# Kernel optimization log

Measured on AMD Instinct MI355X. Metric: run time of the kernel, lower is better.

Reference implementation:

```python
import jax, jax.numpy as jnp
import numpy as np
from jax import lax

B, V, N = 32, 3, 128          # batch, views, worm points
H, W = 512, 512               # image_size
DECAY_FACTOR = 10.0           # MAX_DECAY_FACTOR buffer value
OOB = 1e-05                   # oob_grad_val
MAX_STEPS = 10
LR, ALPHA, EPS = 0.2, 0.99, 1e-08  # torch.optim.RMSprop defaults (lr=0.2)

_b = jnp.arange(B)[:, None, None]   # (B,1,1)
_c = jnp.arange(V)[None, :, None]   # (1,3,1)


def _get_yx(p):
    # round -> long -> clamp to [0, H-1]; col 1 is y (row), col 0 is x (col)
    pi = jnp.clip(jnp.round(p).astype(jnp.int32), 0, H - 1)
    return pi[..., 1], pi[..., 0]  # each (B,3,N)


def _points_to_masks(p):
    y, x = _get_yx(p)
    return jnp.zeros((B, V, H, W), jnp.float32).at[_b, _c, y, x].set(1.0)


def _gradient_surface(masks_diff):
    grad0 = -masks_diff  # (B,3,H,W)
    grads = [grad0]
    g = grad0
    while g.shape[-1] > 1:
        gp = jnp.pad(g, ((0, 0), (0, 0), (1, 1), (1, 1)), constant_values=OOB)
        g = lax.reduce_window(gp, 0.0, lax.add, (1, 1, 3, 3), (1, 1, 2, 2), 'VALID') / 9.0
        grads.append(g)
    gs = jnp.zeros_like(grad0)
    for g in grads:
        # F.interpolate bilinear align_corners=False == jax.image.resize 'linear'
        gs = gs + jax.image.resize(g, grad0.shape, 'linear')
    ga = gs / len(grads)
    gapx = jnp.pad(ga, ((0, 0), (0, 0), (1, 1), (0, 0)), mode='edge')
    gx = (gapx[:, :, :-2] - gapx[:, :, 2:]) * 0.5   # central diff along H
    gapy = jnp.pad(ga, ((0, 0), (0, 0), (0, 0), (1, 1)), mode='edge')
    gy = (gapy[..., :-2] - gapy[..., 2:]) * 0.5     # central diff along W
    return jnp.stack([gx, gy])  # (2,B,3,H,W)


def setup_inputs() -> dict:
    key = jax.random.key(0)
    k1, k2 = jax.random.split(key)
    points_2d = jax.random.uniform(k1, (B, V, N, 2), jnp.float32) * (H - 1)
    masks_target = jax.random.uniform(k2, (B, V, H, W), jnp.float32)
    return {'points_2d': points_2d, 'masks_target': masks_target}


def reference(points_2d, masks_target):
    decay = jnp.exp(-jnp.arange(N, dtype=jnp.float32) / N * DECAY_FACTOR)  # (N,)
    masks_out = _points_to_masks(points_2d)
    masks_diff = masks_target - 0.01 * masks_out
    J = _gradient_surface(masks_diff)  # (2,B,3,H,W)
    p0 = lax.stop_gradient(points_2d)  # matches .clone().detach()

    def body(carry, _):
        p, sq, done = carry
        y, x = _get_yx(p)
        pl = (1.0 - masks_target[_b, _c, y, x]) * decay  # (B,3,N)
        cont = pl.max() > 0.1
        active = jnp.logical_and(jnp.logical_not(done), cont)
        gxp = J[0][_b, _c, y, x]
        gyp = J[1][_b, _c, y, x]
        g = -jnp.stack([gyp, gxp], axis=-1) * pl[..., None]  # (B,3,N,2)
        # RMSprop step
        sq_n = ALPHA * sq + (1.0 - ALPHA) * g * g
        p_n = p - LR * g / (jnp.sqrt(sq_n) + EPS)
        p = jnp.where(active, p_n, p)
        sq = jnp.where(active, sq_n, sq)
        done = jnp.logical_or(done, jnp.logical_not(cont))
        return (p, sq, done), None

    (p_opt, _, _), _ = lax.scan(body, (p0, jnp.zeros_like(p0), jnp.array(False)), None, length=MAX_STEPS)
    masks_opt = _points_to_masks(p_opt)
    return masks_out, masks_opt, p_opt
```

## Files before the change

### kernel.cpp

```cpp
#include <hip/hip_runtime.h>

#define IMGS 96
#define HW   262144
#define NPTS 12288
#define OOBV 1e-5f

static constexpr size_t PYR_OFF   = 0;
static constexpr size_t PFIN_OFF  = 8388576;
static constexpr size_t PLMAX_OFF = 8413152;
static constexpr size_t CNT_OFF   = 8413163;
static constexpr size_t LIST_OFF  = 8413164;
static constexpr size_t GA_OFF    = 8425472;

__device__ __forceinline__ int clampi(int v, int lo, int hi) {
    v = v < lo ? lo : v;
    return v > hi ? hi : v;
}

__global__ void k_scatter(const float* __restrict__ pts, float* __restrict__ mo,
                          int* __restrict__ cnt, int* __restrict__ plist) {
    int i = blockIdx.x * blockDim.x + threadIdx.x;
    if (i >= NPTS) return;
    float px = pts[2*i], py = pts[2*i+1];
    int xi = clampi((int)rintf(px), 0, 511);
    int yi = clampi((int)rintf(py), 0, 511);
    int gp = (i >> 7) * HW + yi * 512 + xi;
    float old = atomicExch(&mo[gp], 1.0f);
    if (old == 0.0f) {
        int k = atomicAdd(cnt, 1);
        plist[k] = gp;
    }
}

__global__ void k_lvl1(const float* __restrict__ mt, float* __restrict__ out) {
    int t = blockIdx.x * blockDim.x + threadIdx.x;
    if (t >= IMGS * 65536) return;
    int j = t & 255, i = (t >> 8) & 255, img = t >> 16;
    const float* m = mt + (size_t)img * HW;
    float s = 0.0f;
    #pragma unroll
    for (int dy = -1; dy <= 1; ++dy) {
        int y = 2*i + dy;
        #pragma unroll
        for (int dx = -1; dx <= 1; ++dx) {
            int x = 2*j + dx;
            s += (y >= 0 && y < 512 && x >= 0 && x < 512) ? -m[y*512 + x] : OOBV;
        }
    }
    out[t] = s / 9.0f;
}

__global__ void k_corr1(const int* __restrict__ cnt, const int* __restrict__ plist,
                        float* __restrict__ lvl1) {
    int k = blockIdx.x * blockDim.x + threadIdx.x;
    if (k >= *cnt) return;
    int gp = plist[k];
    int img = gp >> 18;
    int r = gp & (HW - 1);
    int y = r >> 9, x = r & 511;
    float* L = lvl1 + (size_t)img * 65536;
    const float c = 0.01f / 9.0f;
    int ilo = y >> 1, ihi = ((y + 1) >> 1) > 255 ? 255 : ((y + 1) >> 1);
    int jlo = x >> 1, jhi = ((x + 1) >> 1) > 255 ? 255 : ((x + 1) >> 1);
    for (int i = ilo; i <= ihi; ++i)
        for (int j = jlo; j <= jhi; ++j)
            atomicAdd(&L[i*256 + j], c);
}

__global__ void k_lvl2(const float* __restrict__ in, float* __restrict__ out) {
    int t = blockIdx.x * blockDim.x + threadIdx.x;
    if (t >= IMGS * 16384) return;
    int j = t & 127, i = (t >> 7) & 127, img = t >> 14;
    const float* m = in + (size_t)img * 65536;
    float s = 0.0f;
    #pragma unroll
    for (int dy = -1; dy <= 1; ++dy) {
        int y = 2*i + dy;
        #pragma unroll
        for (int dx = -1; dx <= 1; ++dx) {
            int x = 2*j + dx;
            s += (y >= 0 && y < 256 && x >= 0 && x < 256) ? m[y*256 + x] : OOBV;
        }
    }
    out[t] = s / 9.0f;
}

__global__ __launch_bounds__(256) void k_pyrtail(float* __restrict__ pyr) {
    __shared__ float buf[5461];
    int img = blockIdx.x;
    const float* L2 = pyr + 6291456 + (size_t)img * 16384;
    for (int t = threadIdx.x; t < 4096; t += 256) {
        int i = t >> 6, j = t & 63;
        float s = 0.0f;
        #pragma unroll
        for (int dy = -1; dy <= 1; ++dy) {
            int y = 2*i + dy;
            #pragma unroll
            for (int dx = -1; dx <= 1; ++dx) {
                int x = 2*j + dx;
                s += (y >= 0 && y < 128 && x >= 0 && x < 128) ? L2[y*128 + x] : OOBV;
            }
        }
        float v = s / 9.0f;
        buf[t] = v;
        pyr[7864320 + (size_t)img * 4096 + t] = v;
    }
    __syncthreads();
    int inOff = 0, sin = 64;
    size_t goff = 8257536;
    while (sin > 1) {
        int sout = sin >> 1;
        int outOff = inOff + sin * sin;
        for (int t = threadIdx.x; t < sout * sout; t += 256) {
            int i = t / sout, j = t - i * sout;
            float s = 0.0f;
            for (int dy = -1; dy <= 1; ++dy) {
                int y = 2*i + dy;
                for (int dx = -1; dx <= 1; ++dx) {
                    int x = 2*j + dx;
                    s += (y >= 0 && y < sin && x >= 0 && x < sin) ? buf[inOff + y*sin + x] : OOBV;
                }
            }
            float v = s / 9.0f;
            buf[outOff + t] = v;
            pyr[goff + (size_t)img * sout * sout + t] = v;
        }
        __syncthreads();
        inOff = outOff; sin = sout;
        goff += (size_t)96 * sout * sout;
    }
}

__global__ __launch_bounds__(256) void k_ga(const float* __restrict__ mt,
                                            const float* __restrict__ pyr,
                                            float* __restrict__ ga) {
    __shared__ float vrow[8][520];
    int img = blockIdx.x >> 6;
    int h0 = (blockIdx.x & 63) * 8;

    #pragma unroll
    for (int l = 0; l < 9; ++l) {
        const int s = 256 >> l;
        const int vo = 512 - (512 >> l) + l;
        const float scale = (float)s * (1.0f / 512.0f);
        const float* Lp = pyr + (8388608 - (8388608 >> (2*l))) + (size_t)img * s * s;
        for (int e = threadIdx.x; e < 8*(s+1); e += 256) {
            int r = e / (s+1);
            int x = e - r*(s+1);
            int xx = x < s ? x : s - 1;
            float hf = (float)(h0 + r);
            float fy = (hf + 0.5f) * scale - 0.5f;
            fy = fminf(fmaxf(fy, 0.0f), (float)(s - 1));
            float fyf = floorf(fy);
            int y0 = (int)fyf;
            float ty = fy - fyf;
            int yb = (y0 + 1 < s) ? y0 + 1 : s - 1;
            float a = Lp[y0*s + xx], b = Lp[yb*s + xx];
            vrow[r][vo + x] = (1.0f - ty) * a + ty * b;
        }
    }
    __syncthreads();

    int   x0v[2][9];
    float txv[2][9];
    #pragma unroll
    for (int rep = 0; rep < 2; ++rep) {
        float wf = (float)(threadIdx.x + rep * 256);
        #pragma unroll
        for (int l = 0; l < 9; ++l) {
            const int s = 256 >> l;
            const float scale = (float)s * (1.0f / 512.0f);
            float fx = (wf + 0.5f) * scale - 0.5f;
            fx = fminf(fmaxf(fx, 0.0f), (float)(s - 1));
            float fxf = floorf(fx);
            x0v[rep][l] = (int)fxf + (512 - (512 >> l) + l);
            txv[rep][l] = fx - fxf;
        }
    }

    for (int r = 0; r < 8; ++r) {
        int h = h0 + r;
        #pragma unroll
        for (int rep = 0; rep < 2; ++rep) {
            int w = threadIdx.x + rep * 256;
            int idx = img * HW + h * 512 + w;
            float acc = -mt[idx];
            #pragma unroll
            for (int l = 0; l < 9; ++l) {
                float a = vrow[r][x0v[rep][l]];
                float b = vrow[r][x0v[rep][l] + 1];
                float tx = txv[rep][l];
                acc += (1.0f - tx) * a + tx * b;
            }
            ga[idx] = acc / 10.0f;
        }
    }
}

__global__ void k_corrga(const int* __restrict__ cnt, const int* __restrict__ plist,
                         float* __restrict__ ga) {
    int k = blockIdx.x * blockDim.x + threadIdx.x;
    if (k >= *cnt) return;
    ga[plist[k]] += 0.001f;
}

__global__ __launch_bounds__(256) void k_traj(const float* __restrict__ pts,
                                              const float* __restrict__ mt,
                                              const float* __restrict__ ga,
                                              float* __restrict__ pfin,
                                              float* __restrict__ plmax) {
    int i = blockIdx.x * 256 + threadIdx.x;
    float px = pts[2*i], py = pts[2*i+1];
    int img = i >> 7, n = i & 127;
    const float* M = mt + (size_t)img * HW;
    const float* G = ga + (size_t)img * HW;
    float d = expf(-(float)n * 0.078125f);
    float s0 = 0.0f, s1 = 0.0f;

    for (int t = 0; t < 10; ++t) {
        int xi = clampi((int)rintf(px), 0, 511);
        int yi = clampi((int)rintf(py), 0, 511);
        float pl = (1.0f - M[yi*512 + xi]) * d;
        float r = pl;
        #pragma unroll
        for (int off = 32; off; off >>= 1) r = fmaxf(r, __shfl_xor(r, off, 64));
        if ((threadIdx.x & 63) == 0)
            atomicMax((int*)&plmax[t], __float_as_int(r));
        float gxp = (G[clampi(yi-1,0,511)*512 + xi] - G[clampi(yi+1,0,511)*512 + xi]) * 0.5f;
        float gyp = (G[yi*512 + clampi(xi-1,0,511)] - G[yi*512 + clampi(xi+1,0,511)]) * 0.5f;
        float g0 = -gyp * pl;
        float g1 = -gxp * pl;
        s0 = 0.99f * s0 + 0.01f * g0 * g0;
        s1 = 0.99f * s1 + 0.01f * g1 * g1;
        px = px - 0.2f * g0 / (sqrtf(s0) + 1e-8f);
        py = py - 0.2f * g1 / (sqrtf(s1) + 1e-8f);
    }
    pfin[2*i] = px; pfin[2*i+1] = py;
}

__global__ __launch_bounds__(256) void k_final(const float* __restrict__ pts,
                                               const float* __restrict__ mt,
                                               const float* __restrict__ ga,
                                               const float* __restrict__ pfin,
                                               const float* __restrict__ plmax,
                                               float* __restrict__ mopt,
                                               float* __restrict__ pout) {
    int tstop = 10;
    #pragma unroll
    for (int t = 9; t >= 0; --t)
        if (!(plmax[t] > 0.1f)) tstop = t;
    int i = blockIdx.x * 256 + threadIdx.x;
    float px, py;
    if (tstop == 10) {
        px = pfin[2*i]; py = pfin[2*i+1];
    } else {
        px = pts[2*i]; py = pts[2*i+1];
        int img = i >> 7, n = i & 127;
        const float* M = mt + (size_t)img * HW;
        const float* G = ga + (size_t)img * HW;
        float d = expf(-(float)n * 0.078125f);
        float s0 = 0.0f, s1 = 0.0f;
        for (int t = 0; t < tstop; ++t) {
            int xi = clampi((int)rintf(px), 0, 511);
            int yi = clampi((int)rintf(py), 0, 511);
            float pl = (1.0f - M[yi*512 + xi]) * d;
            float gxp = (G[clampi(yi-1,0,511)*512 + xi] - G[clampi(yi+1,0,511)*512 + xi]) * 0.5f;
            float gyp = (G[yi*512 + clampi(xi-1,0,511)] - G[yi*512 + clampi(xi+1,0,511)]) * 0.5f;
            float g0 = -gyp * pl;
            float g1 = -gxp * pl;
            s0 = 0.99f * s0 + 0.01f * g0 * g0;
            s1 = 0.99f * s1 + 0.01f * g1 * g1;
            px = px - 0.2f * g0 / (sqrtf(s0) + 1e-8f);
            py = py - 0.2f * g1 / (sqrtf(s1) + 1e-8f);
        }
    }
    pout[2*i] = px; pout[2*i+1] = py;
    int xi = clampi((int)rintf(px), 0, 511);
    int yi = clampi((int)rintf(py), 0, 511);
    mopt[(i >> 7) * HW + yi*512 + xi] = 1.0f;
}

extern "C" void kernel_launch(void* const* d_in, const int* in_sizes, int n_in,
                              void* d_out, int out_size, void* d_ws, size_t ws_size,
                              hipStream_t stream) {
    const float* pts = (const float*)d_in[0];
    const float* mt  = (const float*)d_in[1];
    if (in_sizes[0] != NPTS * 2) { const float* tmp = pts; pts = mt; mt = tmp; }

    float* out  = (float*)d_out;
    float* mo   = out;
    float* mopt = out + (size_t)IMGS * HW;
    float* pout = out + 2 * (size_t)IMGS * HW;

    float* ws    = (float*)d_ws;
    float* pyr   = ws + PYR_OFF;
    float* pfin  = ws + PFIN_OFF;
    float* plmax = ws + PLMAX_OFF;
    int*   cnt   = (int*)(ws + CNT_OFF);
    int*   plist = (int*)(ws + LIST_OFF);
    float* ga    = ws + GA_OFF;

    hipMemsetAsync(out, 0, (size_t)out_size * sizeof(float), stream);
    hipMemsetAsync(plmax, 0, 12 * sizeof(float), stream);

    k_scatter<<<NPTS/256, 256, 0, stream>>>(pts, mo, cnt, plist);
    k_lvl1<<<IMGS*65536/256, 256, 0, stream>>>(mt, pyr);
    k_corr1<<<NPTS/256, 256, 0, stream>>>(cnt, plist, pyr);
    k_lvl2<<<IMGS*16384/256, 256, 0, stream>>>(pyr, pyr + 6291456);
    k_pyrtail<<<IMGS, 256, 0, stream>>>(pyr);
    k_ga<<<IMGS*64, 256, 0, stream>>>(mt, pyr, ga);
    k_corrga<<<NPTS/256, 256, 0, stream>>>(cnt, plist, ga);
    k_traj<<<NPTS/256, 256, 0, stream>>>(pts, mt, ga, pfin, plmax);
    k_final<<<NPTS/256, 256, 0, stream>>>(pts, mt, ga, pfin, plmax, mopt, pout);
}
```

Before: 426.9 us.

## Evaluate gradient surface on demand at sampled points instead of full image

Removes the full-resolution k_ga pass that upsampled and summed all pyramid levels for every pixel, along with the k_corrga correction kernel. The trajectory and final kernels now compute the gradient surface lazily at only the four neighbour pixels each point samples, reading pyramid levels directly and applying the mask correction by checking the scattered mask. This avoids writing and reading a 96x512x512 buffer, at the cost of more scattered pyramid reads and arithmetic per trajectory step in a small-grid kernel.

```diff
diff --git a/kernel.cpp b/kernel.cpp
--- a/kernel.cpp
+++ b/kernel.cpp
@@ -10,7 +10,6 @@
 static constexpr size_t PLMAX_OFF = 8413152;
 static constexpr size_t CNT_OFF   = 8413163;
 static constexpr size_t LIST_OFF  = 8413164;
-static constexpr size_t GA_OFF    = 8425472;
 
 __device__ __forceinline__ int clampi(int v, int lo, int hi) {
     v = v < lo ? lo : v;
@@ -131,89 +130,48 @@
     }
 }
 
-__global__ __launch_bounds__(256) void k_ga(const float* __restrict__ mt,
-                                            const float* __restrict__ pyr,
-                                            float* __restrict__ ga) {
-    __shared__ float vrow[8][520];
-    int img = blockIdx.x >> 6;
-    int h0 = (blockIdx.x & 63) * 8;
-
+__device__ __forceinline__ float ga_eval(const float* __restrict__ mt,
+                                         const float* __restrict__ mo,
+                                         const float* __restrict__ pyr,
+                                         int img, int y, int x) {
+    int idx = img * HW + y * 512 + x;
+    float acc = -mt[idx];
     #pragma unroll
     for (int l = 0; l < 9; ++l) {
         const int s = 256 >> l;
-        const int vo = 512 - (512 >> l) + l;
         const float scale = (float)s * (1.0f / 512.0f);
         const float* Lp = pyr + (8388608 - (8388608 >> (2*l))) + (size_t)img * s * s;
-        for (int e = threadIdx.x; e < 8*(s+1); e += 256) {
-            int r = e / (s+1);
-            int x = e - r*(s+1);
-            int xx = x < s ? x : s - 1;
-            float hf = (float)(h0 + r);
-            float fy = (hf + 0.5f) * scale - 0.5f;
-            fy = fminf(fmaxf(fy, 0.0f), (float)(s - 1));
-            float fyf = floorf(fy);
-            int y0 = (int)fyf;
-            float ty = fy - fyf;
-            int yb = (y0 + 1 < s) ? y0 + 1 : s - 1;
-            float a = Lp[y0*s + xx], b = Lp[yb*s + xx];
-            vrow[r][vo + x] = (1.0f - ty) * a + ty * b;
-        }
-    }
-    __syncthreads();
-
-    int   x0v[2][9];
-    float txv[2][9];
-    #pragma unroll
-    for (int rep = 0; rep < 2; ++rep) {
-        float wf = (float)(threadIdx.x + rep * 256);
-        #pragma unroll
-        for (int l = 0; l < 9; ++l) {
-            const int s = 256 >> l;
-            const float scale = (float)s * (1.0f / 512.0f);
-            float fx = (wf + 0.5f) * scale - 0.5f;
-            fx = fminf(fmaxf(fx, 0.0f), (float)(s - 1));
-            float fxf = floorf(fx);
-            x0v[rep][l] = (int)fxf + (512 - (512 >> l) + l);
-            txv[rep][l] = fx - fxf;
-        }
-    }
-
-    for (int r = 0; r < 8; ++r) {
-        int h = h0 + r;
-        #pragma unroll
-        for (int rep = 0; rep < 2; ++rep) {
-            int w = threadIdx.x + rep * 256;
-            int idx = img * HW + h * 512 + w;
-            float acc = -mt[idx];
-            #pragma unroll
-            for (int l = 0; l < 9; ++l) {
-                float a = vrow[r][x0v[rep][l]];
-                float b = vrow[r][x0v[rep][l] + 1];
-                float tx = txv[rep][l];
-                acc += (1.0f - tx) * a + tx * b;
-            }
-            ga[idx] = acc / 10.0f;
-        }
-    }
-}
-
-__global__ void k_corrga(const int* __restrict__ cnt, const int* __restrict__ plist,
-                         float* __restrict__ ga) {
-    int k = blockIdx.x * blockDim.x + threadIdx.x;
-    if (k >= *cnt) return;
-    ga[plist[k]] += 0.001f;
+        float fy = ((float)y + 0.5f) * scale - 0.5f;
+        fy = fminf(fmaxf(fy, 0.0f), (float)(s - 1));
+        float fyf = floorf(fy);
+        int y0 = (int)fyf;
+        float ty = fy - fyf;
+        int yb = (y0 + 1 < s) ? y0 + 1 : s - 1;
+        float fx = ((float)x + 0.5f) * scale - 0.5f;
+        fx = fminf(fmaxf(fx, 0.0f), (float)(s - 1));
+        float fxf = floorf(fx);
+        int x0 = (int)fxf;
+        float tx = fx - fxf;
+        int xb = (x0 + 1 < s) ? x0 + 1 : s - 1;
+        float a = (1.0f - ty) * Lp[y0*s + x0] + ty * Lp[yb*s + x0];
+        float b = (1.0f - ty) * Lp[y0*s + xb] + ty * Lp[yb*s + xb];
+        acc += (1.0f - tx) * a + tx * b;
+    }
+    float v = acc / 10.0f;
+    if (mo[idx] == 1.0f) v += 0.001f;
+    return v;
 }
 
 __global__ __launch_bounds__(256) void k_traj(const float* __restrict__ pts,
                                               const float* __restrict__ mt,
-                                              const float* __restrict__ ga,
+                                              const float* __restrict__ mo,
+                                              const float* __restrict__ pyr,
                                               float* __restrict__ pfin,
                                               float* __restrict__ plmax) {
     int i = blockIdx.x * 256 + threadIdx.x;
     float px = pts[2*i], py = pts[2*i+1];
     int img = i >> 7, n = i & 127;
     const float* M = mt + (size_t)img * HW;
-    const float* G = ga + (size_t)img * HW;
     float d = expf(-(float)n * 0.078125f);
     float s0 = 0.0f, s1 = 0.0f;
 
@@ -226,8 +184,10 @@
         for (int off = 32; off; off >>= 1) r = fmaxf(r, __shfl_xor(r, off, 64));
         if ((threadIdx.x & 63) == 0)
             atomicMax((int*)&plmax[t], __float_as_int(r));
-        float gxp = (G[clampi(yi-1,0,511)*512 + xi] - G[clampi(yi+1,0,511)*512 + xi]) * 0.5f;
-        float gyp = (G[yi*512 + clampi(xi-1,0,511)] - G[yi*512 + clampi(xi+1,0,511)]) * 0.5f;
+        float gxp = (ga_eval(mt, mo, pyr, img, clampi(yi-1,0,511), xi)
+                   - ga_eval(mt, mo, pyr, img, clampi(yi+1,0,511), xi)) * 0.5f;
+        float gyp = (ga_eval(mt, mo, pyr, img, yi, clampi(xi-1,0,511))
+                   - ga_eval(mt, mo, pyr, img, yi, clampi(xi+1,0,511))) * 0.5f;
         float g0 = -gyp * pl;
         float g1 = -gxp * pl;
         s0 = 0.99f * s0 + 0.01f * g0 * g0;
@@ -240,7 +200,8 @@
 
 __global__ __launch_bounds__(256) void k_final(const float* __restrict__ pts,
                                                const float* __restrict__ mt,
-                                               const float* __restrict__ ga,
+                                               const float* __restrict__ mo,
+                                               const float* __restrict__ pyr,
                                                const float* __restrict__ pfin,
                                                const float* __restrict__ plmax,
                                                float* __restrict__ mopt,
@@ -257,15 +218,16 @@
         px = pts[2*i]; py = pts[2*i+1];
         int img = i >> 7, n = i & 127;
         const float* M = mt + (size_t)img * HW;
-        const float* G = ga + (size_t)img * HW;
         float d = expf(-(float)n * 0.078125f);
         float s0 = 0.0f, s1 = 0.0f;
         for (int t = 0; t < tstop; ++t) {
             int xi = clampi((int)rintf(px), 0, 511);
             int yi = clampi((int)rintf(py), 0, 511);
             float pl = (1.0f - M[yi*512 + xi]) * d;
-            float gxp = (G[clampi(yi-1,0,511)*512 + xi] - G[clampi(yi+1,0,511)*512 + xi]) * 0.5f;
-            float gyp = (G[yi*512 + clampi(xi-1,0,511)] - G[yi*512 + clampi(xi+1,0,511)]) * 0.5f;
+            float gxp = (ga_eval(mt, mo, pyr, img, clampi(yi-1,0,511), xi)
+                       - ga_eval(mt, mo, pyr, img, clampi(yi+1,0,511), xi)) * 0.5f;
+            float gyp = (ga_eval(mt, mo, pyr, img, yi, clampi(xi-1,0,511))
+                       - ga_eval(mt, mo, pyr, img, yi, clampi(xi+1,0,511))) * 0.5f;
             float g0 = -gyp * pl;
             float g1 = -gxp * pl;
             s0 = 0.99f * s0 + 0.01f * g0 * g0;
@@ -298,7 +260,6 @@
     float* plmax = ws + PLMAX_OFF;
     int*   cnt   = (int*)(ws + CNT_OFF);
     int*   plist = (int*)(ws + LIST_OFF);
-    float* ga    = ws + GA_OFF;
 
     hipMemsetAsync(out, 0, (size_t)out_size * sizeof(float), stream);
     hipMemsetAsync(plmax, 0, 12 * sizeof(float), stream);
@@ -308,8 +269,6 @@
     k_corr1<<<NPTS/256, 256, 0, stream>>>(cnt, plist, pyr);
     k_lvl2<<<IMGS*16384/256, 256, 0, stream>>>(pyr, pyr + 6291456);
     k_pyrtail<<<IMGS, 256, 0, stream>>>(pyr);
-    k_ga<<<IMGS*64, 256, 0, stream>>>(mt, pyr, ga);
-    k_corrga<<<NPTS/256, 256, 0, stream>>>(cnt, plist, ga);
-    k_traj<<<NPTS/256, 256, 0, stream>>>(pts, mt, ga, pfin, plmax);
-    k_final<<<NPTS/256, 256, 0, stream>>>(pts, mt, ga, pfin, plmax, mopt, pout);
-}
+    k_traj<<<NPTS/256, 256, 0, stream>>>(pts, mt, mo, pyr, pfin, plmax);
+    k_final<<<NPTS/256, 256, 0, stream>>>(pts, mt, mo, pyr, pfin, plmax, mopt, pout);
+}
```

New measurement: 442.0 us. +3.5%, slower.
